# Performance work log

Hardware: AMD Instinct MI355X
Metric: run time of the kernel (lower is better)

Reference implementation:

```python
import jax, jax.numpy as jnp
import numpy as np

N_NODES = 50000
N_EDGES = 800000
N_GRAPHS = 128
IN_DIM = 100
HID = 256
STEPS = 5


def setup_inputs() -> dict:
    key = jax.random.key(0)
    ks = jax.random.split(key, 24)
    s = 0.05
    inp = {
        'x': jax.random.normal(ks[0], (N_NODES, IN_DIM), jnp.float32),
        'edge_index': jax.random.randint(ks[1], (2, N_EDGES), 0, N_NODES, jnp.int32),
        'batch': jnp.sort(jax.random.randint(ks[2], (N_NODES,), 0, N_GRAPHS, jnp.int32)),
        # input projection
        'W_in': jax.random.normal(ks[3], (IN_DIM, HID), jnp.float32) * s,
        'b_in': jnp.zeros((HID,), jnp.float32),
        # GatedGraphConv per-step weights [steps, HID, HID]
        'ggc_w': jax.random.normal(ks[4], (STEPS, HID, HID), jnp.float32) * s,
        # GRUCell params (torch layout: rows = [r, z, n] chunks)
        'W_ih': jax.random.normal(ks[5], (3 * HID, HID), jnp.float32) * s,
        'W_hh': jax.random.normal(ks[6], (3 * HID, HID), jnp.float32) * s,
        'b_ih': jnp.zeros((3 * HID,), jnp.float32),
        'b_hh': jnp.zeros((3 * HID,), jnp.float32),
        # attention MLP: HID -> HID//2 -> 1 (sigmoid)
        'Wa1': jax.random.normal(ks[7], (HID, HID // 2), jnp.float32) * s,
        'ba1': jnp.zeros((HID // 2,), jnp.float32),
        'Wa2': jax.random.normal(ks[8], (HID // 2, 1), jnp.float32) * s,
        'ba2': jnp.zeros((1,), jnp.float32),
        # classifier: 2*HID -> HID -> HID//2 -> 2
        'Wc1': jax.random.normal(ks[9], (2 * HID, HID), jnp.float32) * s,
        'bc1': jnp.zeros((HID,), jnp.float32),
        'Wc2': jax.random.normal(ks[10], (HID, HID // 2), jnp.float32) * s,
        'bc2': jnp.zeros((HID // 2,), jnp.float32),
        'Wc3': jax.random.normal(ks[11], (HID // 2, 2), jnp.float32) * s,
        'bc3': jnp.zeros((2,), jnp.float32),
    }
    return inp


def _forward(x, edge_index, batch, W_in, b_in, ggc_w, W_ih, W_hh, b_ih, b_hh,
             Wa1, ba1, Wa2, ba2, Wc1, bc1, Wc2, bc2, Wc3, bc3):
    src, dst = edge_index[0], edge_index[1]
    # input projection + relu
    h = jax.nn.relu(x @ W_in + b_in)  # [N, HID]

    def ggc_step(h, w):
        m = h @ w                                   # [N, HID]
        agg = jax.ops.segment_sum(m[src], dst, num_segments=N_NODES)  # scatter-add
        gi = agg @ W_ih.T + b_ih                    # [N, 3*HID]
        gh = h @ W_hh.T + b_hh
        i_r, i_z, i_n = jnp.split(gi, 3, axis=-1)
        h_r, h_z, h_n = jnp.split(gh, 3, axis=-1)
        r = jax.nn.sigmoid(i_r + h_r)
        z = jax.nn.sigmoid(i_z + h_z)
        n = jnp.tanh(i_n + r * h_n)
        return (1.0 - z) * n + z * h, None

    h, _ = jax.lax.scan(ggc_step, h, ggc_w)
    h = jax.nn.relu(h)

    # attention weights per node (dropout is identity at eval)
    a = jax.nn.sigmoid(jax.nn.relu(h @ Wa1 + ba1) @ Wa2 + ba2)[:, 0]  # [N]
    wx = h * a[:, None]

    counts = jax.ops.segment_sum(jnp.ones((N_NODES,), h.dtype), batch, num_segments=N_GRAPHS)
    mean_p = jax.ops.segment_sum(wx, batch, num_segments=N_GRAPHS) / jnp.maximum(counts, 1.0)[:, None]
    max_p = jax.ops.segment_max(wx, batch, num_segments=N_GRAPHS)
    max_p = jnp.where(counts[:, None] > 0, max_p, 0.0)
    g = jnp.concatenate([mean_p, max_p], axis=1)  # [G, 2*HID]

    g = jax.nn.relu(g @ Wc1 + bc1)
    g = jax.nn.relu(g @ Wc2 + bc2)
    preds = g @ Wc3 + bc3
    return preds, a


def reference(x, edge_index, batch, W_in, b_in, ggc_w, W_ih, W_hh, b_ih, b_hh,
              Wa1, ba1, Wa2, ba2, Wc1, bc1, Wc2, bc2, Wc3, bc3):
    return _forward(x, edge_index, batch, W_in, b_in, ggc_w, W_ih, W_hh, b_ih, b_hh,
                    Wa1, ba1, Wa2, ba2, Wc1, bc1, Wc2, bc2, Wc3, bc3)
```

## Files before the change

kernel.cpp:

```cpp
#include <hip/hip_runtime.h>
#include <cstddef>

#define NN 50000
#define NE 800000
#define NG 128
#define IND 100
#define HID 256
#define NSTEPS 5
#define PCH 8

typedef __attribute__((ext_vector_type(8))) short bf16x8;
typedef __attribute__((ext_vector_type(4))) float f32x4;

__device__ __forceinline__ float b2f(unsigned h) { return __uint_as_float(h << 16); }
__device__ __forceinline__ unsigned short f2b(float f) {
    unsigned u = __float_as_uint(f);
    unsigned r = (u + 0x7FFFu + ((u >> 16) & 1u)) >> 16;
    return (unsigned short)r;
}
__device__ __forceinline__ float sigm(float x) { return 1.f / (1.f + __expf(-x)); }
__device__ __forceinline__ float tanh_fast(float x) { return 1.f - 2.f / (1.f + __expf(2.f * x)); }

#define LSTR 40
__global__ __launch_bounds__(256) void gemm_bf16(const unsigned short* __restrict__ A,
                                                 const unsigned short* __restrict__ Bt,
                                                 const float* __restrict__ bias, int act,
                                                 unsigned short* __restrict__ C,
                                                 int M, int N, int K)
{
    __shared__ unsigned short As[128 * LSTR];
    __shared__ unsigned short Bs[128 * LSTR];
    const int tid  = threadIdx.x;
    const int row0 = blockIdx.y * 128;
    const int col0 = blockIdx.x * 128;
    const int wave = tid >> 6, lane = tid & 63;
    const int wm = wave >> 1, wn = wave & 1;
    const int lr = lane & 15, q = lane >> 4;
    const int r_st = tid >> 2;
    const int ks   = tid & 3;

    f32x4 acc[4][4];
    #pragma unroll
    for (int i = 0; i < 4; ++i)
        #pragma unroll
        for (int j = 0; j < 4; ++j) acc[i][j] = (f32x4){0.f, 0.f, 0.f, 0.f};

    for (int k0 = 0; k0 < K; k0 += 32) {
        #pragma unroll
        for (int it = 0; it < 2; ++it) {
            int r  = r_st + it * 64;
            int ga = min(row0 + r, M - 1);
            uint4 av = *(const uint4*)(A + (size_t)ga * K + k0 + ks * 8);
            *(uint4*)(As + r * LSTR + ks * 8) = av;
            uint4 bv = *(const uint4*)(Bt + (size_t)(col0 + r) * K + k0 + ks * 8);
            *(uint4*)(Bs + r * LSTR + ks * 8) = bv;
        }
        __syncthreads();
        bf16x8 af[4], bfr[4];
        #pragma unroll
        for (int i = 0; i < 4; ++i)
            af[i]  = *(const bf16x8*)(As + (wm * 64 + i * 16 + lr) * LSTR + q * 8);
        #pragma unroll
        for (int j = 0; j < 4; ++j)
            bfr[j] = *(const bf16x8*)(Bs + (wn * 64 + j * 16 + lr) * LSTR + q * 8);
        #pragma unroll
        for (int i = 0; i < 4; ++i)
            #pragma unroll
            for (int j = 0; j < 4; ++j)
                acc[i][j] = __builtin_amdgcn_mfma_f32_16x16x32_bf16(af[i], bfr[j], acc[i][j], 0, 0, 0);
        __syncthreads();
    }
    #pragma unroll
    for (int i = 0; i < 4; ++i) {
        int rbase = row0 + wm * 64 + i * 16 + q * 4;
        #pragma unroll
        for (int j = 0; j < 4; ++j) {
            int col = col0 + wn * 64 + j * 16 + lr;
            if (col >= N) continue;
            float badd = bias ? bias[col] : 0.f;
            #pragma unroll
            for (int r = 0; r < 4; ++r) {
                int row = rbase + r;
                if (row < M) {
                    float v = acc[i][j][r] + badd;
                    if (act) v = fmaxf(v, 0.f);
                    C[(size_t)row * N + col] = f2b(v);
                }
            }
        }
    }
}

__global__ __launch_bounds__(256, 2) void gru_mfma(const unsigned short* __restrict__ agg,
                                                   const unsigned short* __restrict__ hbf,
                                                   float* __restrict__ h,
                                                   unsigned short* __restrict__ hbfo,
                                                   const unsigned short* __restrict__ Wgi,
                                                   const unsigned short* __restrict__ Wgh,
                                                   const float* __restrict__ bih,
                                                   const float* __restrict__ bhh, int M)
{
    __shared__ unsigned short Sa[64 * LSTR];
    __shared__ unsigned short Sh[64 * LSTR];
    const int tid  = threadIdx.x;
    const int row0 = blockIdx.y * 64;
    const int col0 = blockIdx.x * 64;
    const int wave = tid >> 6, lane = tid & 63;
    const int lr = lane & 15, q = lane >> 4;
    const int cw = col0 + wave * 16;
    const int r_st = tid >> 2, ks = tid & 3;

    f32x4 acc[6][4];
    #pragma unroll
    for (int g = 0; g < 6; ++g)
        #pragma unroll
        for (int i = 0; i < 4; ++i) acc[g][i] = (f32x4){0.f, 0.f, 0.f, 0.f};

    const int ga = min(row0 + r_st, M - 1);
    uint4 pa = *(const uint4*)(agg + (size_t)ga * HID + ks * 8);
    uint4 ph = *(const uint4*)(hbf + (size_t)ga * HID + ks * 8);

    #pragma unroll
    for (int kk = 0; kk < 8; ++kk) {
        const int k0 = kk * 32;
        __syncthreads();
        *(uint4*)(Sa + r_st * LSTR + ks * 8) = pa;
        *(uint4*)(Sh + r_st * LSTR + ks * 8) = ph;
        __syncthreads();
        if (kk < 7) {
            pa = *(const uint4*)(agg + (size_t)ga * HID + k0 + 32 + ks * 8);
            ph = *(const uint4*)(hbf + (size_t)ga * HID + k0 + 32 + ks * 8);
        }
        bf16x8 bf[6];
        #pragma unroll
        for (int g = 0; g < 6; ++g) {
            const unsigned short* W = (g < 3) ? Wgi : Wgh;
            bf[g] = *(const bf16x8*)(W + (size_t)((g % 3) * HID + cw + lr) * HID + k0 + q * 8);
        }
        bf16x8 afa[4], afh[4];
        #pragma unroll
        for (int i = 0; i < 4; ++i) {
            afa[i] = *(const bf16x8*)(Sa + (i * 16 + lr) * LSTR + q * 8);
            afh[i] = *(const bf16x8*)(Sh + (i * 16 + lr) * LSTR + q * 8);
        }
        #pragma unroll
        for (int g = 0; g < 6; ++g)
            #pragma unroll
            for (int i = 0; i < 4; ++i)
                acc[g][i] = __builtin_amdgcn_mfma_f32_16x16x32_bf16(
                    (g < 3) ? afa[i] : afh[i], bf[g], acc[g][i], 0, 0, 0);
    }

    const int cg = cw + lr;
    const float brr = bih[cg]         + bhh[cg];
    const float bzz = bih[HID + cg]   + bhh[HID + cg];
    const float bin = bih[2*HID + cg];
    const float bhn = bhh[2*HID + cg];
    #pragma unroll
    for (int i = 0; i < 4; ++i) {
        #pragma unroll
        for (int r = 0; r < 4; ++r) {
            int row = row0 + i * 16 + q * 4 + r;
            if (row < M) {
                float rr = sigm(acc[0][i][r] + acc[3][i][r] + brr);
                float zz = sigm(acc[1][i][r] + acc[4][i][r] + bzz);
                float nn = tanh_fast(acc[2][i][r] + bin + rr * (acc[5][i][r] + bhn));
                size_t off = (size_t)row * HID + cg;
                float hv = h[off];
                float o = (1.f - zz) * nn + zz * hv;
                h[off] = o;
                hbfo[off] = f2b(o);
            }
        }
    }
}

template<int ACT>
__global__ __launch_bounds__(256) void gemm_kn(const float* __restrict__ A,
                                               const float* __restrict__ B,
                                               const float* __restrict__ bias,
                                               float* __restrict__ C,
                                               int M, int N, int K)
{
    __shared__ float As[64][17];
    __shared__ float Bs[16][65];
    const int tid  = threadIdx.x;
    const int row0 = blockIdx.y * 64;
    const int col0 = blockIdx.x * 64;
    const int tr = tid >> 4, tc = tid & 15;
    const int ar = tid >> 2, akq = tid & 3;
    const int bk = tid >> 4, bj = (tid & 15) << 2;

    float acc[4][4] = {};
    for (int k0 = 0; k0 < K; k0 += 16) {
        float4 av = make_float4(0.f,0.f,0.f,0.f);
        if (row0 + ar < M && (k0 + (akq<<2)) < K)
            av = *(const float4*)(A + (size_t)(row0+ar)*K + k0 + (akq<<2));
        As[ar][(akq<<2)+0] = av.x; As[ar][(akq<<2)+1] = av.y;
        As[ar][(akq<<2)+2] = av.z; As[ar][(akq<<2)+3] = av.w;
        float4 bv = make_float4(0.f,0.f,0.f,0.f);
        if (k0 + bk < K)
            bv = *(const float4*)(B + (size_t)(k0+bk)*N + col0 + bj);
        Bs[bk][bj+0] = bv.x; Bs[bk][bj+1] = bv.y; Bs[bk][bj+2] = bv.z; Bs[bk][bj+3] = bv.w;
        __syncthreads();
        #pragma unroll
        for (int k = 0; k < 16; ++k) {
            float a4[4], b4[4];
            #pragma unroll
            for (int i = 0; i < 4; ++i) a4[i] = As[(tr<<2)+i][k];
            #pragma unroll
            for (int j = 0; j < 4; ++j) b4[j] = Bs[k][(tc<<2)+j];
            #pragma unroll
            for (int i = 0; i < 4; ++i)
                #pragma unroll
                for (int j = 0; j < 4; ++j) acc[i][j] += a4[i]*b4[j];
        }
        __syncthreads();
    }
    #pragma unroll
    for (int i = 0; i < 4; ++i) {
        int row = row0 + (tr<<2) + i;
        if (row >= M) continue;
        #pragma unroll
        for (int j = 0; j < 4; ++j) {
            int col = col0 + (tc<<2) + j;
            float v = acc[i][j];
            if (bias) v += bias[col];
            if (ACT == 1) v = fmaxf(v, 0.f);
            C[(size_t)row*N + col] = v;
        }
    }
}

__global__ void edge_count(const int* __restrict__ dst, int* __restrict__ cnt, int E) {
    int e = blockIdx.x*256 + threadIdx.x;
    if (e < E) atomicAdd(&cnt[dst[e]], 1);
}
__global__ void scan_bsums(const int* __restrict__ cnt, int* __restrict__ bsum, int n) {
    __shared__ int sd[512];
    int tid = threadIdx.x, i = blockIdx.x*512 + tid;
    sd[tid] = (i < n) ? cnt[i] : 0;
    __syncthreads();
    for (int off = 256; off > 0; off >>= 1) {
        if (tid < off) sd[tid] += sd[tid+off];
        __syncthreads();
    }
    if (tid == 0) bsum[blockIdx.x] = sd[0];
}
__global__ void scan_top(int* __restrict__ bsum, int nb) {
    __shared__ int sd[128];
    int tid = threadIdx.x;
    int v = (tid < nb) ? bsum[tid] : 0;
    sd[tid] = v;
    __syncthreads();
    for (int off = 1; off < 128; off <<= 1) {
        int t = (tid >= off) ? sd[tid-off] : 0;
        __syncthreads();
        sd[tid] += t;
        __syncthreads();
    }
    if (tid < nb) bsum[tid] = sd[tid] - v;
}
__global__ void scan_local(const int* __restrict__ cnt, const int* __restrict__ bsum,
                           int* __restrict__ rp, int n) {
    __shared__ int sd[512];
    int tid = threadIdx.x, i = blockIdx.x*512 + tid;
    int v = (i < n) ? cnt[i] : 0;
    sd[tid] = v;
    __syncthreads();
    for (int off = 1; off < 512; off <<= 1) {
        int t = (tid >= off) ? sd[tid-off] : 0;
        __syncthreads();
        sd[tid] += t;
        __syncthreads();
    }
    if (i < n) rp[i] = bsum[blockIdx.x] + sd[tid] - v;
    if (i == n-1) rp[n] = bsum[blockIdx.x] + sd[tid];
}
__global__ void edge_fill(const int* __restrict__ src, const int* __restrict__ dst,
                          const int* __restrict__ rp, int* __restrict__ cur,
                          int* __restrict__ ci, int E) {
    int e = blockIdx.x*256 + threadIdx.x;
    if (e < E) {
        int d = dst[e];
        int pos = rp[d] + atomicAdd(&cur[d], 1);
        ci[pos] = src[e];
    }
}

__global__ void gather_agg(const unsigned short* __restrict__ m, unsigned short* __restrict__ agg,
                           const int* __restrict__ rp, const int* __restrict__ ci, int M)
{
    int node = blockIdx.x*4 + (threadIdx.x >> 6);
    int lane = threadIdx.x & 63;
    if (node >= M) return;
    const int half = lane >> 5;
    const int li   = lane & 31;
    int s = rp[node], e = rp[node+1];
    float a[8] = {0.f,0.f,0.f,0.f,0.f,0.f,0.f,0.f};
    int p = s;
    for (; p + 7 < e; p += 8) {
        int r0 = ci[p + half], r1 = ci[p + 2 + half], r2 = ci[p + 4 + half], r3 = ci[p + 6 + half];
        uint4 v0 = *(const uint4*)(m + (size_t)r0 * HID + li * 8);
        uint4 v1 = *(const uint4*)(m + (size_t)r1 * HID + li * 8);
        uint4 v2 = *(const uint4*)(m + (size_t)r2 * HID + li * 8);
        uint4 v3 = *(const uint4*)(m + (size_t)r3 * HID + li * 8);
        a[0] += b2f(v0.x & 0xffffu) + b2f(v1.x & 0xffffu) + b2f(v2.x & 0xffffu) + b2f(v3.x & 0xffffu);
        a[1] += b2f(v0.x >> 16)     + b2f(v1.x >> 16)     + b2f(v2.x >> 16)     + b2f(v3.x >> 16);
        a[2] += b2f(v0.y & 0xffffu) + b2f(v1.y & 0xffffu) + b2f(v2.y & 0xffffu) + b2f(v3.y & 0xffffu);
        a[3] += b2f(v0.y >> 16)     + b2f(v1.y >> 16)     + b2f(v2.y >> 16)     + b2f(v3.y >> 16);
        a[4] += b2f(v0.z & 0xffffu) + b2f(v1.z & 0xffffu) + b2f(v2.z & 0xffffu) + b2f(v3.z & 0xffffu);
        a[5] += b2f(v0.z >> 16)     + b2f(v1.z >> 16)     + b2f(v2.z >> 16)     + b2f(v3.z >> 16);
        a[6] += b2f(v0.w & 0xffffu) + b2f(v1.w & 0xffffu) + b2f(v2.w & 0xffffu) + b2f(v3.w & 0xffffu);
        a[7] += b2f(v0.w >> 16)     + b2f(v1.w >> 16)     + b2f(v2.w >> 16)     + b2f(v3.w >> 16);
    }
    for (; p + 1 < e; p += 2) {
        int r0 = ci[p + half];
        uint4 v = *(const uint4*)(m + (size_t)r0 * HID + li * 8);
        a[0] += b2f(v.x & 0xffffu); a[1] += b2f(v.x >> 16);
        a[2] += b2f(v.y & 0xffffu); a[3] += b2f(v.y >> 16);
        a[4] += b2f(v.z & 0xffffu); a[5] += b2f(v.z >> 16);
        a[6] += b2f(v.w & 0xffffu); a[7] += b2f(v.w >> 16);
    }
    if (p < e && half == 0) {
        int r0 = ci[p];
        uint4 v = *(const uint4*)(m + (size_t)r0 * HID + li * 8);
        a[0] += b2f(v.x & 0xffffu); a[1] += b2f(v.x >> 16);
        a[2] += b2f(v.y & 0xffffu); a[3] += b2f(v.y >> 16);
        a[4] += b2f(v.z & 0xffffu); a[5] += b2f(v.z >> 16);
        a[6] += b2f(v.w & 0xffffu); a[7] += b2f(v.w >> 16);
    }
    #pragma unroll
    for (int u = 0; u < 8; ++u) a[u] += __shfl_xor(a[u], 32, 64);
    if (half == 0) {
        uint4 o;
        o.x = (unsigned)f2b(a[0]) | ((unsigned)f2b(a[1]) << 16);
        o.y = (unsigned)f2b(a[2]) | ((unsigned)f2b(a[3]) << 16);
        o.z = (unsigned)f2b(a[4]) | ((unsigned)f2b(a[5]) << 16);
        o.w = (unsigned)f2b(a[6]) | ((unsigned)f2b(a[7]) << 16);
        *(uint4*)(agg + (size_t)node * HID + li * 8) = o;
    }
}

__global__ void relu_cvt(float* __restrict__ h, unsigned short* __restrict__ hbf, int n4) {
    int i = blockIdx.x*256 + threadIdx.x;
    if (i >= n4) return;
    float4 v = *((float4*)h + i);
    v.x = fmaxf(v.x,0.f); v.y = fmaxf(v.y,0.f); v.z = fmaxf(v.z,0.f); v.w = fmaxf(v.w,0.f);
    *((float4*)h + i) = v;
    uint2 o;
    o.x = (unsigned)f2b(v.x) | ((unsigned)f2b(v.y) << 16);
    o.y = (unsigned)f2b(v.z) | ((unsigned)f2b(v.w) << 16);
    *((uint2*)hbf + i) = o;
}

__global__ void cvt_f2b4(const float* __restrict__ src, unsigned short* __restrict__ dst, int n4) {
    int i = blockIdx.x*256 + threadIdx.x;
    if (i >= n4) return;
    float4 v = *((const float4*)src + i);
    uint2 o;
    o.x = (unsigned)f2b(v.x) | ((unsigned)f2b(v.y) << 16);
    o.y = (unsigned)f2b(v.z) | ((unsigned)f2b(v.w) << 16);
    *((uint2*)dst + i) = o;
}
__global__ void cvt_elem(const float* __restrict__ src, unsigned short* __restrict__ dst, int n) {
    int i = blockIdx.x*256 + threadIdx.x;
    if (i < n) dst[i] = f2b(src[i]);
}
__global__ void prep_wa1(const float* __restrict__ w, unsigned short* __restrict__ wt) {
    int n = blockIdx.x, k = threadIdx.x;
    wt[(size_t)n*HID + k] = f2b(w[(size_t)k*128 + n]);
}

__global__ void att_sig(const unsigned short* __restrict__ t, const float* __restrict__ Wa2,
                        const float* __restrict__ ba2, float* __restrict__ a, int M)
{
    int node = blockIdx.x*4 + (threadIdx.x >> 6);
    int lane = threadIdx.x & 63;
    if (node >= M) return;
    float s = b2f(t[(size_t)node*128 + lane])*Wa2[lane]
            + b2f(t[(size_t)node*128 + 64 + lane])*Wa2[64+lane];
    #pragma unroll
    for (int off = 32; off > 0; off >>= 1) s += __shfl_down(s, off, 64);
    if (lane == 0) a[node] = 1.f/(1.f+__expf(-(s + ba2[0])));
}

__device__ __forceinline__ int lowerb(const int* arr, int n, int val) {
    int lo = 0, hi = n;
    while (lo < hi) { int mid = (lo+hi)>>1; if (arr[mid] < val) lo = mid+1; else hi = mid; }
    return lo;
}
__global__ void pool_partial(const float* __restrict__ h, const float* __restrict__ a,
                             const int* __restrict__ batch, float* __restrict__ part, int M)
{
    int g = blockIdx.x, c = blockIdx.y, j = threadIdx.x;
    int lo = lowerb(batch, M, g);
    int hi = lowerb(batch, M, g+1);
    int len = hi - lo, per = (len + PCH - 1) / PCH;
    int s = lo + c * per, e = min(s + per, hi);
    float sum = 0.f, mx = 0.f;
    for (int n = s; n < e; ++n) {
        float v = h[(size_t)n*HID + j] * a[n];
        sum += v; mx = fmaxf(mx, v);
    }
    float* pp = part + ((size_t)g*PCH + c) * 512;
    pp[j] = sum; pp[256 + j] = mx;
}
__global__ void pool_final(const float* __restrict__ part, const int* __restrict__ batch,
                           float* __restrict__ gout, int M)
{
    int g = blockIdx.x, j = threadIdx.x;
    float sum = 0.f, mx = 0.f;
    for (int c = 0; c < PCH; ++c) {
        const float* pp = part + ((size_t)g*PCH + c) * 512;
        sum += pp[j];
        mx = fmaxf(mx, pp[256 + j]);
    }
    int lo = lowerb(batch, M, g);
    int hi = lowerb(batch, M, g+1);
    float cnt = (float)(hi - lo);
    gout[(size_t)g*512 + j]       = sum / fmaxf(cnt, 1.f);
    gout[(size_t)g*512 + 256 + j] = mx;
}

__global__ void preds_kernel(const float* __restrict__ g2, const float* __restrict__ W,
                             const float* __restrict__ b, float* __restrict__ out)
{
    int t = threadIdx.x;
    int row = t >> 1, col = t & 1;
    float s = b[col];
    for (int k = 0; k < 128; ++k) s += g2[row*128 + k] * W[k*2 + col];
    out[row*2 + col] = s;
}

extern "C" void kernel_launch(void* const* d_in, const int* in_sizes, int n_in,
                              void* d_out, int out_size, void* d_ws, size_t ws_size,
                              hipStream_t stream)
{
    const float* x     = (const float*)d_in[0];
    const int*   eidx  = (const int*)  d_in[1];
    const int*   batch = (const int*)  d_in[2];
    const float* W_in  = (const float*)d_in[3];
    const float* b_in  = (const float*)d_in[4];
    const float* ggc_w = (const float*)d_in[5];
    const float* W_ih  = (const float*)d_in[6];
    const float* W_hh  = (const float*)d_in[7];
    const float* b_ih  = (const float*)d_in[8];
    const float* b_hh  = (const float*)d_in[9];
    const float* Wa1   = (const float*)d_in[10];
    const float* ba1   = (const float*)d_in[11];
    const float* Wa2   = (const float*)d_in[12];
    const float* ba2   = (const float*)d_in[13];
    const float* Wc1   = (const float*)d_in[14];
    const float* bc1   = (const float*)d_in[15];
    const float* Wc2   = (const float*)d_in[16];
    const float* bc2   = (const float*)d_in[17];
    const float* Wc3   = (const float*)d_in[18];
    const float* bc3   = (const float*)d_in[19];

    float* out  = (float*)d_out;
    float* aout = out + NG*2;

    char* p = (char*)d_ws;
    auto alloc = [&](size_t bytes) -> char* {
        char* r = p; p += (bytes + 255) & ~(size_t)255; return r;
    };
    float*          hf    = (float*)alloc((size_t)NN*HID*4);
    unsigned short* hbfP  = (unsigned short*)alloc((size_t)NN*HID*2);
    unsigned short* hbfQ  = (unsigned short*)alloc((size_t)NN*HID*2);
    unsigned short* aggbf = (unsigned short*)alloc((size_t)NN*HID*2);
    int* row_ptr = (int*)alloc((NN+1)*4);
    int* cursor  = (int*)alloc(NN*4);
    int* col_idx = (int*)alloc((size_t)NE*4);
    int* bsum    = (int*)alloc(128*4);
    unsigned short* wgbf   = (unsigned short*)alloc((size_t)NSTEPS*HID*HID*2);
    unsigned short* WihBf  = (unsigned short*)alloc((size_t)768*HID*2);
    unsigned short* WhhBf  = (unsigned short*)alloc((size_t)768*HID*2);
    unsigned short* WcombT = (unsigned short*)alloc((size_t)NSTEPS*768*HID*2);
    unsigned short* Wa1t   = (unsigned short*)alloc((size_t)128*HID*2);
    float* part = (float*)alloc((size_t)NG*PCH*512*4);
    float* gbuf = (float*)alloc((size_t)NG*2*HID*4);
    float* g1   = (float*)alloc((size_t)NG*HID*4);
    float* g2   = (float*)alloc((size_t)NG*128*4);

    const int* esrc = eidx;
    const int* edst = eidx + NE;
    dim3 blk(256);
    const int NB512 = (NN + 511) / 512;

    hipMemsetAsync(cursor, 0, NN*sizeof(int), stream);
    edge_count<<<NE/256, blk, 0, stream>>>(edst, cursor, NE);
    scan_bsums<<<NB512, 512, 0, stream>>>(cursor, bsum, NN);
    scan_top<<<1, 128, 0, stream>>>(bsum, NB512);
    scan_local<<<NB512, 512, 0, stream>>>(cursor, bsum, row_ptr, NN);
    hipMemsetAsync(cursor, 0, NN*sizeof(int), stream);
    edge_fill<<<NE/256, blk, 0, stream>>>(esrc, edst, row_ptr, cursor, col_idx, NE);

    cvt_elem<<<(NSTEPS*HID*HID + 255)/256, blk, 0, stream>>>(ggc_w, wgbf, NSTEPS*HID*HID);
    cvt_elem<<<768, blk, 0, stream>>>(W_ih, WihBf, 768*HID);
    cvt_elem<<<768, blk, 0, stream>>>(W_hh, WhhBf, 768*HID);
    prep_wa1<<<128, blk, 0, stream>>>(Wa1, Wa1t);
    for (int s = 0; s < NSTEPS; ++s)
        gemm_bf16<<<dim3(2, 6), blk, 0, stream>>>(
            WihBf, wgbf + (size_t)s*HID*HID, nullptr, 0,
            WcombT + (size_t)s*768*HID, 768, HID, HID);

    gemm_kn<1><<<dim3(HID/64, (NN+63)/64), blk, 0, stream>>>(x, W_in, b_in, hf, NN, HID, IND);
    cvt_f2b4<<<(NN*HID/4 + 255)/256, blk, 0, stream>>>(hf, hbfP, NN*HID/4);

    unsigned short* hbf  = hbfP;
    unsigned short* hbfn = hbfQ;
    const int MB64 = (NN + 63) / 64;
    for (int s = 0; s < NSTEPS; ++s) {
        gather_agg<<<NN/4, blk, 0, stream>>>(hbf, aggbf, row_ptr, col_idx, NN);
        gru_mfma<<<dim3(HID/64, MB64), blk, 0, stream>>>(
            aggbf, hbf, hf, hbfn, WcombT + (size_t)s*768*HID, WhhBf, b_ih, b_hh, NN);
        unsigned short* t0 = hbf; hbf = hbfn; hbfn = t0;
    }

    relu_cvt<<<(NN*HID/4 + 255)/256, blk, 0, stream>>>(hf, hbf, NN*HID/4);

    unsigned short* tbuf = aggbf;
    gemm_bf16<<<dim3(1, (NN+127)/128), blk, 0, stream>>>(hbf, Wa1t, ba1, 1, tbuf, NN, 128, HID);
    att_sig<<<NN/4, blk, 0, stream>>>(tbuf, Wa2, ba2, aout, NN);

    pool_partial<<<dim3(NG, PCH), blk, 0, stream>>>(hf, aout, batch, part, NN);
    pool_final<<<NG, blk, 0, stream>>>(part, batch, gbuf, NN);

    gemm_kn<1><<<dim3(HID/64, (NG+63)/64), blk, 0, stream>>>(gbuf, Wc1, bc1, g1, NG, HID, 2*HID);
    gemm_kn<1><<<dim3(2,      (NG+63)/64), blk, 0, stream>>>(g1,   Wc2, bc2, g2, NG, 128, HID);
    preds_kernel<<<1, blk, 0, stream>>>(g2, Wc3, bc3, out);
}
```

Measured before the change: 1.355 ms.

## Prefetch GRU operands deeper, fuse final relu, batch weight-combine GEMMs

The GRU MFMA kernel now prefetches activation chunks three K-steps ahead in registers and double-buffers the weight fragments one step ahead, to hide global load latency behind the MFMAs. The standalone relu_cvt pass is removed and the ReLU is applied in the last GRU step's epilogue, saving a full read and write of the hidden state. The five per-step weight-combine GEMMs become one launch using blockIdx.z. The cost is more live registers in gru_mfma, which runs with launch bounds (256, 2) and could spill or lose occupancy.

After: 1.518 ms. +12.0%, slower.

```diff
diff --git a/kernel.cpp b/kernel.cpp
--- a/kernel.cpp
+++ b/kernel.cpp
@@ -26,8 +26,11 @@
                                                  const unsigned short* __restrict__ Bt,
                                                  const float* __restrict__ bias, int act,
                                                  unsigned short* __restrict__ C,
-                                                 int M, int N, int K)
-{
+                                                 int M, int N, int K,
+                                                 size_t btz, size_t cz)
+{
+    Bt += (size_t)blockIdx.z * btz;
+    C  += (size_t)blockIdx.z * cz;
     __shared__ unsigned short As[128 * LSTR];
     __shared__ unsigned short Bs[128 * LSTR];
     const int tid  = threadIdx.x;
@@ -98,7 +101,8 @@
                                                    const unsigned short* __restrict__ Wgi,
                                                    const unsigned short* __restrict__ Wgh,
                                                    const float* __restrict__ bih,
-                                                   const float* __restrict__ bhh, int M)
+                                                   const float* __restrict__ bhh,
+                                                   int M, int dorelu)
 {
     __shared__ unsigned short Sa[64 * LSTR];
     __shared__ unsigned short Sh[64 * LSTR];
@@ -117,25 +121,40 @@
         for (int i = 0; i < 4; ++i) acc[g][i] = (f32x4){0.f, 0.f, 0.f, 0.f};
 
     const int ga = min(row0 + r_st, M - 1);
-    uint4 pa = *(const uint4*)(agg + (size_t)ga * HID + ks * 8);
-    uint4 ph = *(const uint4*)(hbf + (size_t)ga * HID + ks * 8);
+    const size_t abase = (size_t)ga * HID + ks * 8;
+
+    uint4 ca[3], ch[3];
+    #pragma unroll
+    for (int c = 0; c < 3; ++c) {
+        ca[c] = *(const uint4*)(agg + abase + c * 32);
+        ch[c] = *(const uint4*)(hbf + abase + c * 32);
+    }
+    const unsigned short* wp[6];
+    #pragma unroll
+    for (int g = 0; g < 6; ++g) {
+        const unsigned short* W = (g < 3) ? Wgi : Wgh;
+        wp[g] = W + (size_t)((g % 3) * HID + cw + lr) * HID + q * 8;
+    }
+    bf16x8 wcur[6];
+    #pragma unroll
+    for (int g = 0; g < 6; ++g) wcur[g] = *(const bf16x8*)(wp[g]);
 
     #pragma unroll
     for (int kk = 0; kk < 8; ++kk) {
-        const int k0 = kk * 32;
-        __syncthreads();
-        *(uint4*)(Sa + r_st * LSTR + ks * 8) = pa;
-        *(uint4*)(Sh + r_st * LSTR + ks * 8) = ph;
-        __syncthreads();
+        const int slot = kk % 3;
+        __syncthreads();
+        *(uint4*)(Sa + r_st * LSTR + ks * 8) = ca[slot];
+        *(uint4*)(Sh + r_st * LSTR + ks * 8) = ch[slot];
+        __syncthreads();
+        if (kk + 3 < 8) {
+            ca[slot] = *(const uint4*)(agg + abase + (kk + 3) * 32);
+            ch[slot] = *(const uint4*)(hbf + abase + (kk + 3) * 32);
+        }
+        bf16x8 wnxt[6];
         if (kk < 7) {
-            pa = *(const uint4*)(agg + (size_t)ga * HID + k0 + 32 + ks * 8);
-            ph = *(const uint4*)(hbf + (size_t)ga * HID + k0 + 32 + ks * 8);
-        }
-        bf16x8 bf[6];
-        #pragma unroll
-        for (int g = 0; g < 6; ++g) {
-            const unsigned short* W = (g < 3) ? Wgi : Wgh;
-            bf[g] = *(const bf16x8*)(W + (size_t)((g % 3) * HID + cw + lr) * HID + k0 + q * 8);
+            #pragma unroll
+            for (int g = 0; g < 6; ++g)
+                wnxt[g] = *(const bf16x8*)(wp[g] + (kk + 1) * 32);
         }
         bf16x8 afa[4], afh[4];
         #pragma unroll
@@ -148,7 +167,11 @@
             #pragma unroll
             for (int i = 0; i < 4; ++i)
                 acc[g][i] = __builtin_amdgcn_mfma_f32_16x16x32_bf16(
-                    (g < 3) ? afa[i] : afh[i], bf[g], acc[g][i], 0, 0, 0);
+                    (g < 3) ? afa[i] : afh[i], wcur[g], acc[g][i], 0, 0, 0);
+        if (kk < 7) {
+            #pragma unroll
+            for (int g = 0; g < 6; ++g) wcur[g] = wnxt[g];
+        }
     }
 
     const int cg = cw + lr;
@@ -168,6 +191,7 @@
                 size_t off = (size_t)row * HID + cg;
                 float hv = h[off];
                 float o = (1.f - zz) * nn + zz * hv;
+                if (dorelu) o = fmaxf(o, 0.f);
                 h[off] = o;
                 hbfo[off] = f2b(o);
             }
@@ -342,18 +366,6 @@
     }
 }
 
-__global__ void relu_cvt(float* __restrict__ h, unsigned short* __restrict__ hbf, int n4) {
-    int i = blockIdx.x*256 + threadIdx.x;
-    if (i >= n4) return;
-    float4 v = *((float4*)h + i);
-    v.x = fmaxf(v.x,0.f); v.y = fmaxf(v.y,0.f); v.z = fmaxf(v.z,0.f); v.w = fmaxf(v.w,0.f);
-    *((float4*)h + i) = v;
-    uint2 o;
-    o.x = (unsigned)f2b(v.x) | ((unsigned)f2b(v.y) << 16);
-    o.y = (unsigned)f2b(v.z) | ((unsigned)f2b(v.w) << 16);
-    *((uint2*)hbf + i) = o;
-}
-
 __global__ void cvt_f2b4(const float* __restrict__ src, unsigned short* __restrict__ dst, int n4) {
     int i = blockIdx.x*256 + threadIdx.x;
     if (i >= n4) return;
@@ -500,10 +512,9 @@
     cvt_elem<<<768, blk, 0, stream>>>(W_ih, WihBf, 768*HID);
     cvt_elem<<<768, blk, 0, stream>>>(W_hh, WhhBf, 768*HID);
     prep_wa1<<<128, blk, 0, stream>>>(Wa1, Wa1t);
-    for (int s = 0; s < NSTEPS; ++s)
-        gemm_bf16<<<dim3(2, 6), blk, 0, stream>>>(
-            WihBf, wgbf + (size_t)s*HID*HID, nullptr, 0,
-            WcombT + (size_t)s*768*HID, 768, HID, HID);
+    gemm_bf16<<<dim3(2, 6, NSTEPS), blk, 0, stream>>>(
+        WihBf, wgbf, nullptr, 0, WcombT, 768, HID, HID,
+        (size_t)HID*HID, (size_t)768*HID);
 
     gemm_kn<1><<<dim3(HID/64, (NN+63)/64), blk, 0, stream>>>(x, W_in, b_in, hf, NN, HID, IND);
     cvt_f2b4<<<(NN*HID/4 + 255)/256, blk, 0, stream>>>(hf, hbfP, NN*HID/4);
@@ -514,14 +525,13 @@
     for (int s = 0; s < NSTEPS; ++s) {
         gather_agg<<<NN/4, blk, 0, stream>>>(hbf, aggbf, row_ptr, col_idx, NN);
         gru_mfma<<<dim3(HID/64, MB64), blk, 0, stream>>>(
-            aggbf, hbf, hf, hbfn, WcombT + (size_t)s*768*HID, WhhBf, b_ih, b_hh, NN);
+            aggbf, hbf, hf, hbfn, WcombT + (size_t)s*768*HID, WhhBf, b_ih, b_hh,
+            NN, (s == NSTEPS-1) ? 1 : 0);
         unsigned short* t0 = hbf; hbf = hbfn; hbfn = t0;
     }
 
-    relu_cvt<<<(NN*HID/4 + 255)/256, blk, 0, stream>>>(hf, hbf, NN*HID/4);
-
     unsigned short* tbuf = aggbf;
-    gemm_bf16<<<dim3(1, (NN+127)/128), blk, 0, stream>>>(hbf, Wa1t, ba1, 1, tbuf, NN, 128, HID);
+    gemm_bf16<<<dim3(1, (NN+127)/128), blk, 0, stream>>>(hbf, Wa1t, ba1, 1, tbuf, NN, 128, HID, 0, 0);
     att_sig<<<NN/4, blk, 0, stream>>>(tbuf, Wa2, ba2, aout, NN);
 
     pool_partial<<<dim3(NG, PCH), blk, 0, stream>>>(hf, aout, batch, part, NN);
```
